# Kernel optimization log

Hardware: AMD Instinct MI355X
Metric: run time of the kernel (lower is better)

## Reference

```python
import jax, jax.numpy as jnp
import numpy as np

B, N, H, E = 4, 256, 128, 16
EIN = 2 * H + 1 + E  # edge MLP input dim
LN_EPS = 1e-6  # flax nnx.LayerNorm default epsilon


def layer_norm(x, scale, bias):
    m = jnp.mean(x, axis=-1, keepdims=True)
    v = jnp.var(x, axis=-1, keepdims=True)
    return (x - m) * jax.lax.rsqrt(v + LN_EPS) * scale + bias


def mlp2(x, W1, b1, s, sb, W2, b2):
    # Linear -> LayerNorm -> ReLU -> Linear (dropout deterministic)
    h = jax.nn.relu(layer_norm(x @ W1 + b1, s, sb))
    return h @ W2 + b2


def setup_inputs() -> dict:
    key = jax.random.key(0)
    ks = jax.random.split(key, 24)

    def lin(k, fi, fo):
        k1, k2 = jax.random.split(k)
        W = jax.random.normal(k1, (fi, fo), jnp.float32) / np.sqrt(fi)
        b = jnp.zeros((fo,), jnp.float32)
        return W, b

    We1, be1 = lin(ks[0], EIN, H)
    We2, be2 = lin(ks[1], H, H)
    Wa, ba = lin(ks[2], EIN, 1)
    Wn1, bn1 = lin(ks[3], 2 * H, H)
    Wn2, bn2 = lin(ks[4], H, H)
    Wc1, bc1 = lin(ks[5], H, H)
    Wc2, bc2 = lin(ks[6], H, 1)

    return {
        "node_features": jax.random.normal(ks[7], (B, N, H), jnp.float32),
        "coordinates": jax.random.normal(ks[8], (B, N, 3), jnp.float32),
        "edge_features": jax.random.normal(ks[9], (B, N, N, E), jnp.float32),
        "mask": jnp.ones((B, N), jnp.float32),
        "We1": We1, "be1": be1,
        "ln_e_s": jnp.ones((H,), jnp.float32), "ln_e_b": jnp.zeros((H,), jnp.float32),
        "We2": We2, "be2": be2,
        "Wa": Wa, "ba": ba,
        "Wn1": Wn1, "bn1": bn1,
        "ln_n_s": jnp.ones((H,), jnp.float32), "ln_n_b": jnp.zeros((H,), jnp.float32),
        "Wn2": Wn2, "bn2": bn2,
        "Wc1": Wc1, "bc1": bc1,
        "ln_c_s": jnp.ones((H,), jnp.float32), "ln_c_b": jnp.zeros((H,), jnp.float32),
        "Wc2": Wc2, "bc2": bc2,
        "edge_index": jax.random.randint(ks[10], (B, N, N), 0, 2, jnp.int32),
    }


def reference(node_features, coordinates, edge_features, mask,
              We1, be1, ln_e_s, ln_e_b, We2, be2,
              Wa, ba,
              Wn1, bn1, ln_n_s, ln_n_b, Wn2, bn2,
              Wc1, bc1, ln_c_s, ln_c_b, Wc2, bc2,
              edge_index):
    b, n, h = node_features.shape
    rel_pos = coordinates[:, :, None, :] - coordinates[:, None, :, :]  # [B,N,N,3]
    d2 = jnp.sum(rel_pos ** 2, axis=-1, keepdims=True)                 # [B,N,N,1]

    node_i = jnp.broadcast_to(node_features[:, :, None, :], (b, n, n, h))
    node_j = jnp.broadcast_to(node_features[:, None, :, :], (b, n, n, h))
    edge_inputs = jnp.concatenate([node_i, node_j, d2, edge_features], axis=-1)  # [B,N,N,EIN]

    edge_messages = mlp2(edge_inputs, We1, be1, ln_e_s, ln_e_b, We2, be2)  # [B,N,N,H]
    new_edge_features = edge_messages

    att = jax.nn.sigmoid(edge_inputs @ Wa + ba)  # [B,N,N,1]
    adj = edge_index[..., None].astype(edge_messages.dtype)  # [B,N,N,1]
    msg_mask = (mask[:, :, None] * mask[:, None, :])[..., None]

    edge_messages = edge_messages * att * adj * msg_mask
    node_messages = jnp.sum(edge_messages, axis=2)  # [B,N,H]

    node_inputs = jnp.concatenate([node_features, node_messages], axis=-1)
    new_node_features = mlp2(node_inputs, Wn1, bn1, ln_n_s, ln_n_b, Wn2, bn2)

    coord_messages = mlp2(node_messages, Wc1, bc1, ln_c_s, ln_c_b, Wc2, bc2)  # [B,N,1]

    norm = jnp.sqrt(d2 + 1e-8)
    normalized_rel_pos = rel_pos / norm
    coord_update_dir = jnp.sum(normalized_rel_pos * att * adj, axis=2)  # [B,N,3]
    coord_updates = coord_update_dir * coord_messages * mask[:, :, None]
    new_coordinates = coordinates + coord_updates

    new_node_features = node_features + new_node_features  # residual
    return (new_node_features, new_coordinates, new_edge_features)
```

## Files before the change

kernel.cpp:

```cpp
#include <hip/hip_runtime.h>
#include <hip/hip_bf16.h>


typedef unsigned short ushort_t;
typedef __attribute__((ext_vector_type(8))) short short8;
typedef __attribute__((ext_vector_type(4))) float f32x4;

__device__ __forceinline__ ushort_t f2bf(float f) {
  unsigned int x = __builtin_bit_cast(unsigned int, f);
  x += 0x7fffu + ((x >> 16) & 1u);
  return (ushort_t)(x >> 16);
}
__device__ __forceinline__ float bf2f(ushort_t u) {
  unsigned int x = ((unsigned int)u) << 16;
  return __builtin_bit_cast(float, x);
}
__device__ __forceinline__ bool looks_bf16(const float* mk) {
  return __builtin_bit_cast(unsigned int, mk[0]) == 0x3F803F80u;
}

__global__ void k_sent777(float* out0) { out0[threadIdx.x] = 777.f; }

__global__ __launch_bounds__(128)
void k_pre(const float* nf, const float* We1, const float* be1,
           const float* Wa, const float* mk,
           float* pre_i, float* pre_j, float* api, float* apj, float* sent) {
  int r = blockIdx.x, t = threadIdx.x;
  if (looks_bf16(mk)) {
    if (r == 0) sent[t] = 555.f;
    return;
  }
  __shared__ float nfv[128];
  __shared__ float red[4];
  nfv[t] = nf[(size_t)r * 128 + t];
  __syncthreads();
  float s1 = be1[t], s2 = 0.f;
  for (int c = 0; c < 128; ++c) {
    float x = nfv[c];
    s1 += x * We1[c * 128 + t];
    s2 += x * We1[(128 + c) * 128 + t];
  }
  pre_i[(size_t)r * 128 + t] = s1;
  pre_j[(size_t)r * 128 + t] = s2;
  float t1 = nfv[t] * Wa[t];
  float t2 = nfv[t] * Wa[128 + t];
#pragma unroll
  for (int o = 32; o > 0; o >>= 1) { t1 += __shfl_down(t1, o); t2 += __shfl_down(t2, o); }
  if ((t & 63) == 0) { red[(t >> 6) * 2] = t1; red[(t >> 6) * 2 + 1] = t2; }
  __syncthreads();
  if (t == 0) { api[r] = red[0] + red[2]; apj[r] = red[1] + red[3]; }
}

__global__ __launch_bounds__(256)
void k_pack(const float* We2, ushort_t* bpack) {
  int t = blockIdx.x * 256 + threadIdx.x;
  if (t >= 2048) return;
  int ks = t >> 9, nt = (t >> 6) & 7, l = t & 63;
  int kb = ks * 32 + (l >> 4) * 8, col = nt * 16 + (l & 15);
#pragma unroll
  for (int e = 0; e < 8; ++e) bpack[t * 8 + e] = f2bf(We2[(kb + e) * 128 + col]);
}

__global__ __launch_bounds__(128)
void k_edge(const float* co, const float* efo, const float* mk,
            const float* We1, const float* be2, const float* Wa, const float* ba,
            const float* lnes, const float* lneb, const int* eidx,
            const float* pre_i, const float* pre_j, const float* api, const float* apj,
            const ushort_t* bpack, float* oute, float* nm2, float* cd2) {
  __shared__ __align__(16) ushort_t h1s[128 * 136];
  __shared__ float wef[17 * 128];
  __shared__ float preI[128];
  __shared__ float lns[128], lnb[128];
  __shared__ float attw[128];
  __shared__ float nmp[2][128];
  __shared__ float cred[2][3];

  if (looks_bf16(mk)) return;

  const int bx = blockIdx.x;
  const int r = bx >> 1, half = bx & 1;
  const int b = r >> 8;
  const int t = threadIdx.x;
  const int lane = t & 63, w = t >> 6;

  for (int q = t; q < 17 * 128; q += 128) {
    int e = q >> 7, c = q & 127;
    int row = (e < 16) ? (257 + e) : 256;
    wef[q] = We1[row * 128 + c];
  }
  preI[t] = pre_i[(size_t)r * 128 + t];
  lns[t] = lnes[t];
  lnb[t] = lneb[t];
  __syncthreads();

  const int j = half * 128 + t;
  const int gj = b * 256 + j;

  float dx = co[r * 3 + 0] - co[gj * 3 + 0];
  float dy = co[r * 3 + 1] - co[gj * 3 + 1];
  float dz = co[r * 3 + 2] - co[gj * 3 + 2];
  float d2 = dx * dx + dy * dy + dz * dz;

  float efv[17];
  {
    const float* efp = efo + ((size_t)r * 256 + j) * 16;
    f32x4 e0 = *reinterpret_cast<const f32x4*>(efp);
    f32x4 e1 = *reinterpret_cast<const f32x4*>(efp + 4);
    f32x4 e2 = *reinterpret_cast<const f32x4*>(efp + 8);
    f32x4 e3 = *reinterpret_cast<const f32x4*>(efp + 12);
#pragma unroll
    for (int x = 0; x < 4; ++x) {
      efv[x] = e0[x]; efv[4 + x] = e1[x]; efv[8 + x] = e2[x]; efv[12 + x] = e3[x];
    }
  }
  efv[16] = d2;

  float a = api[r] + apj[gj] + ba[0] + d2 * Wa[256];
#pragma unroll
  for (int e = 0; e < 16; ++e) a += efv[e] * Wa[257 + e];
  float att = 1.f / (1.f + __expf(-a));
  float aw = att * (float)eidx[(size_t)r * 256 + j];
  attw[t] = aw * mk[r] * mk[gj];
  float invn = rsqrtf(d2 + 1e-8f);
  float c0 = dx * invn * aw, c1 = dy * invn * aw, c2 = dz * invn * aw;
#pragma unroll
  for (int o = 32; o > 0; o >>= 1) {
    c0 += __shfl_down(c0, o); c1 += __shfl_down(c1, o); c2 += __shfl_down(c2, o);
  }
  if (lane == 0) { cred[w][0] = c0; cred[w][1] = c1; cred[w][2] = c2; }

  float s = 0.f, ss = 0.f;
  ushort_t* hrow = h1s + t * 136;
  const float* pjrow = pre_j + (size_t)gj * 128;
#pragma unroll
  for (int q = 0; q < 16; ++q) {
    f32x4 pj0 = *reinterpret_cast<const f32x4*>(pjrow + q * 8);
    f32x4 pj1 = *reinterpret_cast<const f32x4*>(pjrow + q * 8 + 4);
    float hv[8];
#pragma unroll
    for (int x = 0; x < 8; ++x)
      hv[x] = preI[q * 8 + x] + (x < 4 ? pj0[x] : pj1[x - 4]);
#pragma unroll
    for (int e = 0; e < 17; ++e) {
      float ev = efv[e];
#pragma unroll
      for (int x = 0; x < 8; ++x) hv[x] += ev * wef[e * 128 + q * 8 + x];
    }
    short8 pk;
#pragma unroll
    for (int x = 0; x < 8; ++x) {
      s += hv[x]; ss += hv[x] * hv[x];
      pk[x] = (short)f2bf(hv[x]);
    }
    *reinterpret_cast<short8*>(hrow + q * 8) = pk;
  }
  float mean = s * (1.f / 128.f);
  float var = fmaxf(ss * (1.f / 128.f) - mean * mean, 0.f);
  float rsv = rsqrtf(var + 1e-6f);
#pragma unroll
  for (int q = 0; q < 16; ++q) {
    short8 pk = *reinterpret_cast<short8*>(hrow + q * 8);
    short8 op;
#pragma unroll
    for (int x = 0; x < 8; ++x) {
      float xv = bf2f((ushort_t)pk[x]);
      float gv = (xv - mean) * rsv * lns[q * 8 + x] + lnb[q * 8 + x];
      op[x] = (short)f2bf(fmaxf(gv, 0.f));
    }
    *reinterpret_cast<short8*>(hrow + q * 8) = op;
  }
  __syncthreads();

  if (t == 0) {
#pragma unroll
    for (int d = 0; d < 3; ++d)
      cd2[(size_t)(half * 1024 + r) * 3 + d] = cred[0][d] + cred[1][d];
  }

  f32x4 acc[4][8];
#pragma unroll
  for (int mt = 0; mt < 4; ++mt)
#pragma unroll
    for (int nt = 0; nt < 8; ++nt) acc[mt][nt] = (f32x4){0.f, 0.f, 0.f, 0.f};

  const short* h1p = reinterpret_cast<const short*>(h1s);
#pragma unroll
  for (int ks = 0; ks < 4; ++ks) {
    short8 bfr[8];
#pragma unroll
    for (int nt = 0; nt < 8; ++nt)
      bfr[nt] = *reinterpret_cast<const short8*>(bpack + (((ks * 8 + nt) * 64 + lane) * 8));
#pragma unroll
    for (int mt = 0; mt < 4; ++mt) {
      short8 afr = *reinterpret_cast<const short8*>(
          h1p + (w * 64 + mt * 16 + (lane & 15)) * 136 + ks * 32 + ((lane >> 4) * 8));
#pragma unroll
      for (int nt = 0; nt < 8; ++nt)
        acc[mt][nt] = __builtin_amdgcn_mfma_f32_16x16x32_bf16(afr, bfr[nt], acc[mt][nt], 0, 0, 0);
    }
  }

  float be2v[8], pnm[8];
#pragma unroll
  for (int nt = 0; nt < 8; ++nt) { be2v[nt] = be2[nt * 16 + (lane & 15)]; pnm[nt] = 0.f; }
  const size_t obase = ((size_t)r * 256 + half * 128) * 128;
#pragma unroll
  for (int mt = 0; mt < 4; ++mt)
#pragma unroll
    for (int r4 = 0; r4 < 4; ++r4) {
      int row = w * 64 + mt * 16 + (lane >> 4) * 4 + r4;
      float wgt = attw[row];
#pragma unroll
      for (int nt = 0; nt < 8; ++nt) {
        float val = acc[mt][nt][r4] + be2v[nt];
        oute[obase + (size_t)row * 128 + nt * 16 + (lane & 15)] = val;
        pnm[nt] += val * wgt;
      }
    }
#pragma unroll
  for (int nt = 0; nt < 8; ++nt) {
    pnm[nt] += __shfl_xor(pnm[nt], 16);
    pnm[nt] += __shfl_xor(pnm[nt], 32);
  }
  if (lane < 16)
#pragma unroll
    for (int nt = 0; nt < 8; ++nt) nmp[w][nt * 16 + lane] = pnm[nt];
  __syncthreads();
  nm2[(size_t)(half * 1024 + r) * 128 + t] = nmp[0][t] + nmp[1][t];
}

__device__ __forceinline__ float bsum128(float v, float* red, int t) {
#pragma unroll
  for (int o = 32; o > 0; o >>= 1) v += __shfl_down(v, o);
  __syncthreads();
  if ((t & 63) == 0) red[t >> 6] = v;
  __syncthreads();
  return red[0] + red[1];
}

__global__ __launch_bounds__(128)
void k_node(const float* nf, const float* co, const float* mk,
            const float* Wn1, const float* bn1, const float* lnns, const float* lnnb,
            const float* Wn2, const float* bn2,
            const float* Wc1, const float* bc1, const float* lncs, const float* lncb,
            const float* Wc2, const float* bc2,
            const float* nm2, const float* cd2,
            float* out0, float* out1) {
  if (looks_bf16(mk)) return;
  int r = blockIdx.x, t = threadIdx.x;
  __shared__ float nin[256];
  __shared__ float hf[128];
  __shared__ float red[2];
  float nfv = nf[(size_t)r * 128 + t];
  float nmv = nm2[(size_t)r * 128 + t] + nm2[(size_t)(1024 + r) * 128 + t];
  nin[t] = nfv; nin[128 + t] = nmv;
  __syncthreads();
  float s1 = bn1[t];
  for (int c = 0; c < 256; ++c) s1 += nin[c] * Wn1[c * 128 + t];
  float mean = bsum128(s1, red, t) * (1.f / 128.f);
  float var = fmaxf(bsum128(s1 * s1, red, t) * (1.f / 128.f) - mean * mean, 0.f);
  float hv = (s1 - mean) * rsqrtf(var + 1e-6f) * lnns[t] + lnnb[t];
  hv = fmaxf(hv, 0.f);
  hf[t] = hv;
  __syncthreads();
  float o1 = bn2[t] + nfv;
  for (int c = 0; c < 128; ++c) o1 += hf[c] * Wn2[c * 128 + t];
  out0[(size_t)r * 128 + t] = o1;
  float g = bc1[t];
  for (int c = 0; c < 128; ++c) g += nin[128 + c] * Wc1[c * 128 + t];
  float gm = bsum128(g, red, t) * (1.f / 128.f);
  float gv = fmaxf(bsum128(g * g, red, t) * (1.f / 128.f) - gm * gm, 0.f);
  float gh = fmaxf((g - gm) * rsqrtf(gv + 1e-6f) * lncs[t] + lncb[t], 0.f);
  float cm = bsum128(gh * Wc2[t], red, t) + bc2[0];
  if (t < 3) {
    float cd = cd2[(size_t)r * 3 + t] + cd2[(size_t)(1024 + r) * 3 + t];
    float nc = co[(size_t)r * 3 + t] + cd * cm * mk[r];
    out1[(size_t)r * 3 + t] = nc;
  }
}

extern "C" void kernel_launch(void* const* d_in, const int* in_sizes, int n_in,
                              void* d_out, int out_size, void* d_ws, size_t ws_size,
                              hipStream_t stream) {
  const float* nf   = (const float*)d_in[0];
  const float* co   = (const float*)d_in[1];
  const float* efo  = (const float*)d_in[2];
  const float* mk   = (const float*)d_in[3];
  const float* We1  = (const float*)d_in[4];
  const float* be1  = (const float*)d_in[5];
  const float* lnes = (const float*)d_in[6];
  const float* lneb = (const float*)d_in[7];
  const float* We2  = (const float*)d_in[8];
  const float* be2  = (const float*)d_in[9];
  const float* Wa   = (const float*)d_in[10];
  const float* ba   = (const float*)d_in[11];
  const float* Wn1  = (const float*)d_in[12];
  const float* bn1  = (const float*)d_in[13];
  const float* lnns = (const float*)d_in[14];
  const float* lnnb = (const float*)d_in[15];
  const float* Wn2  = (const float*)d_in[16];
  const float* bn2  = (const float*)d_in[17];
  const float* Wc1  = (const float*)d_in[18];
  const float* bc1  = (const float*)d_in[19];
  const float* lncs = (const float*)d_in[20];
  const float* lncb = (const float*)d_in[21];
  const float* Wc2  = (const float*)d_in[22];
  const float* bc2  = (const float*)d_in[23];
  const int* eidx   = (const int*)d_in[24];

  float* out0 = (float*)d_out;
  float* out1 = out0 + 131072;
  float* oute = out1 + 3072;

  const size_t need = (size_t)(131072 + 131072 + 1024 + 1024 + 262144 + 6144) * 4 + 16384 * 2;
  if (ws_size < need) {
    k_sent777<<<1, 128, 0, stream>>>(out0);
    return;
  }
  float* ws    = (float*)d_ws;
  float* pre_i = ws;
  float* pre_j = pre_i + 131072;
  float* api   = pre_j + 131072;
  float* apj   = api + 1024;
  float* nm2   = apj + 1024;
  float* cd2   = nm2 + 262144;
  ushort_t* bpack = (ushort_t*)(cd2 + 6144);

  k_pre<<<1024, 128, 0, stream>>>(nf, We1, be1, Wa, mk, pre_i, pre_j, api, apj, out0);
  k_pack<<<8, 256, 0, stream>>>(We2, bpack);
  k_edge<<<2048, 128, 0, stream>>>(co, efo, mk, We1, be2, Wa, ba, lnes, lneb, eidx,
                                   pre_i, pre_j, api, apj, bpack, oute, nm2, cd2);
  k_node<<<1024, 128, 0, stream>>>(nf, co, mk, Wn1, bn1, lnns, lnnb, Wn2, bn2,
                                   Wc1, bc1, lncs, lncb, Wc2, bc2, nm2, cd2, out0, out1);
}
```

Baseline: 109.1 us.

## Split each edge row across two threads and four MFMA waves in k_edge

k_edge now runs 256 threads per block instead of 128. Each edge row's 128-channel first-layer computation is split into two 64-channel halves, with LayerNorm statistics combined through shared memory. The pre-LN values now stay in fp32 registers instead of taking a bf16 round trip through LDS. The second-layer MFMA GEMM is spread over four waves of 32 rows each rather than two waves of 64, so more warps are available to hide memory latency. The bf16 input-detection checks and the sentinel output path are removed, and the larger per-thread register array may limit occupancy.

New measurement: 93.02 us. 14.8% less time.

```diff
diff --git a/kernel.cpp b/kernel.cpp
--- a/kernel.cpp
+++ b/kernel.cpp
@@ -11,25 +11,13 @@
   x += 0x7fffu + ((x >> 16) & 1u);
   return (ushort_t)(x >> 16);
 }
-__device__ __forceinline__ float bf2f(ushort_t u) {
-  unsigned int x = ((unsigned int)u) << 16;
-  return __builtin_bit_cast(float, x);
-}
-__device__ __forceinline__ bool looks_bf16(const float* mk) {
-  return __builtin_bit_cast(unsigned int, mk[0]) == 0x3F803F80u;
-}
 
 __global__ void k_sent777(float* out0) { out0[threadIdx.x] = 777.f; }
 
 __global__ __launch_bounds__(128)
 void k_pre(const float* nf, const float* We1, const float* be1,
-           const float* Wa, const float* mk,
-           float* pre_i, float* pre_j, float* api, float* apj, float* sent) {
+           const float* Wa, float* pre_i, float* pre_j, float* api, float* apj) {
   int r = blockIdx.x, t = threadIdx.x;
-  if (looks_bf16(mk)) {
-    if (r == 0) sent[t] = 555.f;
-    return;
-  }
   __shared__ float nfv[128];
   __shared__ float red[4];
   nfv[t] = nf[(size_t)r * 128 + t];
@@ -61,7 +49,7 @@
   for (int e = 0; e < 8; ++e) bpack[t * 8 + e] = f2bf(We2[(kb + e) * 128 + col]);
 }
 
-__global__ __launch_bounds__(128)
+__global__ __launch_bounds__(256)
 void k_edge(const float* co, const float* efo, const float* mk,
             const float* We1, const float* be2, const float* Wa, const float* ba,
             const float* lnes, const float* lneb, const int* eidx,
@@ -69,13 +57,11 @@
             const ushort_t* bpack, float* oute, float* nm2, float* cd2) {
   __shared__ __align__(16) ushort_t h1s[128 * 136];
   __shared__ float wef[17 * 128];
-  __shared__ float preI[128];
   __shared__ float lns[128], lnb[128];
   __shared__ float attw[128];
-  __shared__ float nmp[2][128];
+  __shared__ float lnS[256], lnSS[256];
+  __shared__ float nmp[4][128];
   __shared__ float cred[2][3];
-
-  if (looks_bf16(mk)) return;
 
   const int bx = blockIdx.x;
   const int r = bx >> 1, half = bx & 1;
@@ -83,17 +69,17 @@
   const int t = threadIdx.x;
   const int lane = t & 63, w = t >> 6;
 
-  for (int q = t; q < 17 * 128; q += 128) {
+  for (int q = t; q < 17 * 128; q += 256) {
     int e = q >> 7, c = q & 127;
     int row = (e < 16) ? (257 + e) : 256;
     wef[q] = We1[row * 128 + c];
   }
-  preI[t] = pre_i[(size_t)r * 128 + t];
-  lns[t] = lnes[t];
-  lnb[t] = lneb[t];
-  __syncthreads();
-
-  const int j = half * 128 + t;
+  if (t < 128) { lns[t] = lnes[t]; }
+  else { lnb[t - 128] = lneb[t - 128]; }
+  __syncthreads();
+
+  const int jr = t & 127, ch = t >> 7;
+  const int j = half * 128 + jr;
   const int gj = b * 256 + j;
 
   float dx = co[r * 3 + 0] - co[gj * 3 + 0];
@@ -115,59 +101,53 @@
   }
   efv[16] = d2;
 
-  float a = api[r] + apj[gj] + ba[0] + d2 * Wa[256];
-#pragma unroll
-  for (int e = 0; e < 16; ++e) a += efv[e] * Wa[257 + e];
-  float att = 1.f / (1.f + __expf(-a));
-  float aw = att * (float)eidx[(size_t)r * 256 + j];
-  attw[t] = aw * mk[r] * mk[gj];
-  float invn = rsqrtf(d2 + 1e-8f);
-  float c0 = dx * invn * aw, c1 = dy * invn * aw, c2 = dz * invn * aw;
-#pragma unroll
-  for (int o = 32; o > 0; o >>= 1) {
-    c0 += __shfl_down(c0, o); c1 += __shfl_down(c1, o); c2 += __shfl_down(c2, o);
-  }
-  if (lane == 0) { cred[w][0] = c0; cred[w][1] = c1; cred[w][2] = c2; }
-
+  if (ch == 0) {
+    float a = api[r] + apj[gj] + ba[0] + d2 * Wa[256];
+#pragma unroll
+    for (int e = 0; e < 16; ++e) a += efv[e] * Wa[257 + e];
+    float att = 1.f / (1.f + __expf(-a));
+    float aw = att * (float)eidx[(size_t)r * 256 + j];
+    attw[jr] = aw * mk[r] * mk[gj];
+    float invn = rsqrtf(d2 + 1e-8f);
+    float c0 = dx * invn * aw, c1 = dy * invn * aw, c2 = dz * invn * aw;
+#pragma unroll
+    for (int o = 32; o > 0; o >>= 1) {
+      c0 += __shfl_down(c0, o); c1 += __shfl_down(c1, o); c2 += __shfl_down(c2, o);
+    }
+    if (lane == 0) { cred[w][0] = c0; cred[w][1] = c1; cred[w][2] = c2; }
+  }
+
+  const int cbase = ch * 64;
+  const f32x4* pi4 = reinterpret_cast<const f32x4*>(pre_i + (size_t)r * 128 + cbase);
+  const f32x4* pj4 = reinterpret_cast<const f32x4*>(pre_j + (size_t)gj * 128 + cbase);
+  const f32x4* wef4 = reinterpret_cast<const f32x4*>(wef);
+  float h[64];
   float s = 0.f, ss = 0.f;
-  ushort_t* hrow = h1s + t * 136;
-  const float* pjrow = pre_j + (size_t)gj * 128;
-#pragma unroll
-  for (int q = 0; q < 16; ++q) {
-    f32x4 pj0 = *reinterpret_cast<const f32x4*>(pjrow + q * 8);
-    f32x4 pj1 = *reinterpret_cast<const f32x4*>(pjrow + q * 8 + 4);
-    float hv[8];
-#pragma unroll
-    for (int x = 0; x < 8; ++x)
-      hv[x] = preI[q * 8 + x] + (x < 4 ? pj0[x] : pj1[x - 4]);
-#pragma unroll
-    for (int e = 0; e < 17; ++e) {
-      float ev = efv[e];
-#pragma unroll
-      for (int x = 0; x < 8; ++x) hv[x] += ev * wef[e * 128 + q * 8 + x];
-    }
+#pragma unroll
+  for (int c4 = 0; c4 < 16; ++c4) {
+    f32x4 v = pi4[c4] + pj4[c4];
+#pragma unroll
+    for (int e = 0; e < 17; ++e) v += efv[e] * wef4[e * 32 + (cbase >> 2) + c4];
+#pragma unroll
+    for (int x = 0; x < 4; ++x) { h[c4 * 4 + x] = v[x]; s += v[x]; ss += v[x] * v[x]; }
+  }
+  lnS[t] = s; lnSS[t] = ss;
+  __syncthreads();
+  float st = s + lnS[t ^ 128], sst = ss + lnSS[t ^ 128];
+  float mean = st * (1.f / 128.f);
+  float var = fmaxf(sst * (1.f / 128.f) - mean * mean, 0.f);
+  float rsv = rsqrtf(var + 1e-6f);
+  ushort_t* hrow = h1s + jr * 136 + cbase;
+#pragma unroll
+  for (int q8 = 0; q8 < 8; ++q8) {
     short8 pk;
 #pragma unroll
     for (int x = 0; x < 8; ++x) {
-      s += hv[x]; ss += hv[x] * hv[x];
-      pk[x] = (short)f2bf(hv[x]);
-    }
-    *reinterpret_cast<short8*>(hrow + q * 8) = pk;
-  }
-  float mean = s * (1.f / 128.f);
-  float var = fmaxf(ss * (1.f / 128.f) - mean * mean, 0.f);
-  float rsv = rsqrtf(var + 1e-6f);
-#pragma unroll
-  for (int q = 0; q < 16; ++q) {
-    short8 pk = *reinterpret_cast<short8*>(hrow + q * 8);
-    short8 op;
-#pragma unroll
-    for (int x = 0; x < 8; ++x) {
-      float xv = bf2f((ushort_t)pk[x]);
-      float gv = (xv - mean) * rsv * lns[q * 8 + x] + lnb[q * 8 + x];
-      op[x] = (short)f2bf(fmaxf(gv, 0.f));
-    }
-    *reinterpret_cast<short8*>(hrow + q * 8) = op;
+      int c = q8 * 8 + x;
+      float gv = (h[c] - mean) * rsv * lns[cbase + c] + lnb[cbase + c];
+      pk[x] = (short)f2bf(fmaxf(gv, 0.f));
+    }
+    *reinterpret_cast<short8*>(hrow + q8 * 8) = pk;
   }
   __syncthreads();
 
@@ -177,9 +157,9 @@
       cd2[(size_t)(half * 1024 + r) * 3 + d] = cred[0][d] + cred[1][d];
   }
 
-  f32x4 acc[4][8];
-#pragma unroll
-  for (int mt = 0; mt < 4; ++mt)
+  f32x4 acc[2][8];
+#pragma unroll
+  for (int mt = 0; mt < 2; ++mt)
 #pragma unroll
     for (int nt = 0; nt < 8; ++nt) acc[mt][nt] = (f32x4){0.f, 0.f, 0.f, 0.f};
 
@@ -191,9 +171,9 @@
     for (int nt = 0; nt < 8; ++nt)
       bfr[nt] = *reinterpret_cast<const short8*>(bpack + (((ks * 8 + nt) * 64 + lane) * 8));
 #pragma unroll
-    for (int mt = 0; mt < 4; ++mt) {
+    for (int mt = 0; mt < 2; ++mt) {
       short8 afr = *reinterpret_cast<const short8*>(
-          h1p + (w * 64 + mt * 16 + (lane & 15)) * 136 + ks * 32 + ((lane >> 4) * 8));
+          h1p + (w * 32 + mt * 16 + (lane & 15)) * 136 + ks * 32 + ((lane >> 4) * 8));
 #pragma unroll
       for (int nt = 0; nt < 8; ++nt)
         acc[mt][nt] = __builtin_amdgcn_mfma_f32_16x16x32_bf16(afr, bfr[nt], acc[mt][nt], 0, 0, 0);
@@ -205,10 +185,10 @@
   for (int nt = 0; nt < 8; ++nt) { be2v[nt] = be2[nt * 16 + (lane & 15)]; pnm[nt] = 0.f; }
   const size_t obase = ((size_t)r * 256 + half * 128) * 128;
 #pragma unroll
-  for (int mt = 0; mt < 4; ++mt)
+  for (int mt = 0; mt < 2; ++mt)
 #pragma unroll
     for (int r4 = 0; r4 < 4; ++r4) {
-      int row = w * 64 + mt * 16 + (lane >> 4) * 4 + r4;
+      int row = w * 32 + mt * 16 + (lane >> 4) * 4 + r4;
       float wgt = attw[row];
 #pragma unroll
       for (int nt = 0; nt < 8; ++nt) {
@@ -226,7 +206,8 @@
 #pragma unroll
     for (int nt = 0; nt < 8; ++nt) nmp[w][nt * 16 + lane] = pnm[nt];
   __syncthreads();
-  nm2[(size_t)(half * 1024 + r) * 128 + t] = nmp[0][t] + nmp[1][t];
+  if (t < 128)
+    nm2[(size_t)(half * 1024 + r) * 128 + t] = nmp[0][t] + nmp[1][t] + nmp[2][t] + nmp[3][t];
 }
 
 __device__ __forceinline__ float bsum128(float v, float* red, int t) {
@@ -246,7 +227,6 @@
             const float* Wc2, const float* bc2,
             const float* nm2, const float* cd2,
             float* out0, float* out1) {
-  if (looks_bf16(mk)) return;
   int r = blockIdx.x, t = threadIdx.x;
   __shared__ float nin[256];
   __shared__ float hf[128];
@@ -326,9 +306,9 @@
   float* cd2   = nm2 + 262144;
   ushort_t* bpack = (ushort_t*)(cd2 + 6144);
 
-  k_pre<<<1024, 128, 0, stream>>>(nf, We1, be1, Wa, mk, pre_i, pre_j, api, apj, out0);
+  k_pre<<<1024, 128, 0, stream>>>(nf, We1, be1, Wa, pre_i, pre_j, api, apj);
   k_pack<<<8, 256, 0, stream>>>(We2, bpack);
-  k_edge<<<2048, 128, 0, stream>>>(co, efo, mk, We1, be2, Wa, ba, lnes, lneb, eidx,
+  k_edge<<<2048, 256, 0, stream>>>(co, efo, mk, We1, be2, Wa, ba, lnes, lneb, eidx,
                                    pre_i, pre_j, api, apj, bpack, oute, nm2, cd2);
   k_node<<<1024, 128, 0, stream>>>(nf, co, mk, Wn1, bn1, lnns, lnnb, Wn2, bn2,
                                    Wc1, bc1, lncs, lncb, Wc2, bc2, nm2, cd2, out0, out1);
```
